# Kernel tuning notes

Hardware: AMD Instinct MI355X
Metric: run time of the kernel (lower is better)

The kernel has to match this reference:

```python
import jax, jax.numpy as jnp
import numpy as np

EMBED_DIM = 2048
NUM_HEADS = 16
HEAD_DIM = EMBED_DIM // NUM_HEADS  # 128
EPS = 1e-12  # F.normalize default eps


def setup_inputs() -> dict:
    key = jax.random.key(0)
    k1, k2, k3 = jax.random.split(key, 3)
    x = jax.random.normal(k1, (4, 2048, EMBED_DIM), dtype=jnp.float32)
    # nn.Linear(embed_dim, 3*embed_dim): weight [3E, E], bias [3E]
    W = jax.random.normal(k2, (3 * EMBED_DIM, EMBED_DIM), dtype=jnp.float32) * (EMBED_DIM ** -0.5)
    b = jax.random.normal(k3, (3 * EMBED_DIM,), dtype=jnp.float32) * 0.02
    return {"x": x, "W": W, "b": b}


def _l2_normalize(t):
    # matches F.normalize(p=2, dim=-1): t / max(||t||, eps)
    n = jnp.sqrt(jnp.sum(t * t, axis=-1, keepdims=True))
    return t / jnp.maximum(n, EPS)


def reference(x, W, b):
    B, L, E = x.shape
    H, HD = NUM_HEADS, HEAD_DIM
    y = x @ W.T + b  # [B, L, 3E]
    # rearrange '... l (h c) -> ... h l c' with c = 3*HD, then chunk into q,k,v
    y = y.reshape(B, L, H, 3, HD)
    q = jnp.transpose(y[..., 0, :], (0, 2, 1, 3))  # [B, H, L, HD]
    k = jnp.transpose(y[..., 1, :], (0, 2, 1, 3))
    v = jnp.transpose(y[..., 2, :], (0, 2, 1, 3))
    q = _l2_normalize(q)
    k = _l2_normalize(k)
    # cosine attention, scale=1, non-causal, no mask
    scores = jnp.einsum('bhld,bhmd->bhlm', q, k)
    attn = jax.nn.softmax(scores, axis=-1)
    out = jnp.einsum('bhlm,bhmd->bhld', attn, v)  # [B, H, L, HD]
    return jnp.transpose(out, (0, 2, 1, 3)).reshape(B, L, E)
```

## Files before the change

kernel.cpp:

```cpp
#include <hip/hip_runtime.h>
#include <hip/hip_bf16.h>

typedef __bf16 bf16_t;
typedef __bf16 bf16x8 __attribute__((ext_vector_type(8)));
typedef __bf16 bf16x4 __attribute__((ext_vector_type(4)));
typedef __bf16 bf16x2 __attribute__((ext_vector_type(2)));
typedef float f32x4 __attribute__((ext_vector_type(4)));

#define MFMA16(a,b,c) __builtin_amdgcn_mfma_f32_16x16x32_bf16((a),(b),(c),0,0,0)
#define AS3(p) ((__attribute__((address_space(3))) void*)(p))
#define AS1(p) ((const __attribute__((address_space(1))) void*)(p))

constexpr int B_ = 4, L_ = 2048, E_ = 2048, H_ = 16, HD_ = 128;
constexpr size_t QK_ELEMS = (size_t)B_ * H_ * L_ * HD_;
constexpr size_t NX = (size_t)B_ * L_ * E_;
constexpr size_t NW = (size_t)3 * E_ * E_;

__global__ __launch_bounds__(256) void cvt(
    const float* __restrict__ X, const float* __restrict__ W, bf16_t* __restrict__ dst)
{
  size_t e = ((size_t)blockIdx.x * 256 + threadIdx.x) * 4;
  f32x4 v = (e < NX) ? *(const f32x4*)&X[e] : *(const f32x4*)&W[e - NX];
  bf16x4 o;
  for (int u = 0; u < 4; ++u) o[u] = (__bf16)v[u];
  *(bf16x4*)&dst[e] = o;
}

__global__ __launch_bounds__(256) void gemm_qkv(
    const bf16_t* __restrict__ Xb, const bf16_t* __restrict__ Wb, const float* __restrict__ bias,
    bf16_t* __restrict__ q, bf16_t* __restrict__ k, bf16_t* __restrict__ vT)
{
  __shared__ alignas(16) bf16_t As[2][128 * 32];
  __shared__ alignas(16) bf16_t Bs[2][128 * 32];
  const int tid = threadIdx.x;
  const int wave = tid >> 6, lane = tid & 63;
  const int wm = wave >> 1, wn = wave & 1;
  const int m0 = blockIdx.y * 128, n0 = blockIdx.x * 128;

  const int sr = lane & 15, sq8 = (lane >> 4) * 8;
  const bf16_t* gA = &Xb[(size_t)(m0 + wave * 32 + sr) * E_ + sq8];
  const bf16_t* gB = &Wb[(size_t)(n0 + wave * 32 + sr) * E_ + sq8];
  bf16_t* lA = &As[0][wave * 1024];
  bf16_t* lB = &Bs[0][wave * 1024];

#define STAGE(c, k0) do { \
    __builtin_amdgcn_global_load_lds(AS1(gA + (k0)),           AS3(lA + (c) * 4096),       16, 0, 0); \
    __builtin_amdgcn_global_load_lds(AS1(gA + 16 * E_ + (k0)), AS3(lA + (c) * 4096 + 512), 16, 0, 0); \
    __builtin_amdgcn_global_load_lds(AS1(gB + (k0)),           AS3(lB + (c) * 4096),       16, 0, 0); \
    __builtin_amdgcn_global_load_lds(AS1(gB + 16 * E_ + (k0)), AS3(lB + (c) * 4096 + 512), 16, 0, 0); \
  } while (0)

  const f32x4 fzero = {0.f, 0.f, 0.f, 0.f};
  f32x4 acc[4][4];
  for (int i = 0; i < 4; ++i)
    for (int j = 0; j < 4; ++j) acc[i][j] = fzero;

  STAGE(0, 0);
  __syncthreads();
  int cur = 0;
  for (int t = 0; t < 64; ++t) {
    if (t < 63) STAGE(cur ^ 1, (t + 1) * 32);
    bf16x8 af[4], bfr[4];
    for (int mt = 0; mt < 4; ++mt) af[mt]  = *(const bf16x8*)&As[cur][(wm * 4 + mt) * 512 + lane * 8];
    for (int nt = 0; nt < 4; ++nt) bfr[nt] = *(const bf16x8*)&Bs[cur][(wn * 4 + nt) * 512 + lane * 8];
    __builtin_amdgcn_s_setprio(1);
    for (int mt = 0; mt < 4; ++mt)
      for (int nt = 0; nt < 4; ++nt)
        acc[mt][nt] = MFMA16(af[mt], bfr[nt], acc[mt][nt]);
    __builtin_amdgcn_s_setprio(0);
    __syncthreads();
    cur ^= 1;
  }
#undef STAGE

  const int b  = m0 >> 11;
  const int l0 = m0 & (L_ - 1);
  const int h  = n0 / 384;
  const int which = (n0 % 384) >> 7;
  const int rlane = (lane >> 4) << 2;
  const int clane = lane & 15;

  float bcol[4];
  for (int nt = 0; nt < 4; ++nt)
    bcol[nt] = bias[n0 + wn * 64 + nt * 16 + clane];

  if (which < 2) {
    float* NormS = (float*)&As[0][0];
    for (int mt = 0; mt < 4; ++mt)
      for (int r = 0; r < 4; ++r) {
        float sq = 0.f;
        for (int nt = 0; nt < 4; ++nt) {
          float v = acc[mt][nt][r] + bcol[nt];
          acc[mt][nt][r] = v;
          sq += v * v;
        }
        for (int off = 8; off; off >>= 1) sq += __shfl_xor(sq, off);
        if (clane == 0) NormS[(wm * 64 + mt * 16 + rlane + r) * 2 + wn] = sq;
      }
    __syncthreads();
    float invn[4][4];
    for (int mt = 0; mt < 4; ++mt)
      for (int r = 0; r < 4; ++r) {
        int ll = wm * 64 + mt * 16 + rlane + r;
        float tot = NormS[ll * 2] + NormS[ll * 2 + 1];
        invn[mt][r] = 1.0f / fmaxf(sqrtf(tot), 1e-12f);
      }
    bf16_t* base = ((which == 0) ? q : k) + ((size_t)(b * H_ + h) * L_) * HD_;
    for (int mt = 0; mt < 4; ++mt)
      for (int r = 0; r < 4; ++r) {
        int l = l0 + wm * 64 + mt * 16 + rlane + r;
        bf16_t* rowp = base + (size_t)l * HD_;
        for (int nt = 0; nt < 4; ++nt) {
          int hd = wn * 64 + nt * 16 + clane;
          rowp[hd] = (__bf16)(acc[mt][nt][r] * invn[mt][r]);
        }
      }
  } else {
    bf16_t* base = vT + ((size_t)(b * H_ + h) * HD_) * L_;
    for (int mt = 0; mt < 4; ++mt)
      for (int r = 0; r < 4; ++r) {
        int l = l0 + wm * 64 + mt * 16 + rlane + r;
        for (int nt = 0; nt < 4; ++nt) {
          int hd = wn * 64 + nt * 16 + clane;
          base[(size_t)hd * L_ + l] = (__bf16)(acc[mt][nt][r] + bcol[nt]);
        }
      }
  }
}

__device__ __forceinline__ int swz128(int r, int c) {
  return r * 128 + ((((c >> 3) ^ (r & 15)) & 15) << 3) + (c & 7);
}
__device__ __forceinline__ int swz64(int r, int c) {
  return r * 64 + ((((c >> 3) ^ (r & 7)) & 7) << 3) + (c & 7);
}

__global__ __launch_bounds__(256) void attn(
    const bf16_t* __restrict__ q, const bf16_t* __restrict__ k,
    const bf16_t* __restrict__ vT, float* __restrict__ out)
{
  __shared__ alignas(16) bf16_t Ks[64 * 128];
  __shared__ alignas(16) bf16_t Vts[128 * 64];
  __shared__ alignas(16) bf16_t Ps[128 * 64];

  const int tid = threadIdx.x, wave = tid >> 6, lane = tid & 63;
  const int bh = blockIdx.y;
  const int q0 = blockIdx.x * 128;
  const int rowf = lane & 15, kq8 = (lane >> 4) * 8;

  const bf16_t* qbase = q + ((size_t)bh * L_ + q0) * HD_;
  const bf16_t* kbh = k + (size_t)bh * L_ * HD_;
  const bf16_t* vbh = vT + (size_t)bh * HD_ * L_;

  bf16x8 qf[4][2];
  for (int kk4 = 0; kk4 < 4; ++kk4)
    for (int mt = 0; mt < 2; ++mt)
      qf[kk4][mt] = *(const bf16x8*)&qbase[(size_t)(wave * 32 + mt * 16 + rowf) * HD_ + kk4 * 32 + kq8];

  const f32x4 fzero = {0.f, 0.f, 0.f, 0.f};
  f32x4 o[2][8];
  for (int mt = 0; mt < 2; ++mt)
    for (int nt = 0; nt < 8; ++nt) o[mt][nt] = fzero;
  float lrow[2][4];
  for (int mt = 0; mt < 2; ++mt)
    for (int r = 0; r < 4; ++r) lrow[mt][r] = 0.f;

  bf16x8 kreg[4], vreg[4];

  for (int i = 0; i < 4; ++i) {
    int e = (i * 256 + tid) * 8;
    kreg[i] = *(const bf16x8*)&kbh[e];
  }
  for (int i = 0; i < 4; ++i) {
    int e = (i * 256 + tid) * 8;
    int d = e >> 6, c = e & 63;
    vreg[i] = *(const bf16x8*)&vbh[(size_t)d * L_ + c];
  }
  for (int i = 0; i < 4; ++i) {
    int e = (i * 256 + tid) * 8;
    *(bf16x8*)&Ks[swz128(e >> 7, e & 127)] = kreg[i];
  }
  for (int i = 0; i < 4; ++i) {
    int e = (i * 256 + tid) * 8;
    int d = e >> 6, c = e & 63;
    *(bf16x8*)&Vts[swz64(d, c)] = vreg[i];
  }
  __syncthreads();

  for (int j0 = 0; j0 < L_; j0 += 64) {
    const bool more = (j0 + 64 < L_);
    if (more) {
      const int jn = j0 + 64;
      for (int i = 0; i < 4; ++i) {
        int e = (i * 256 + tid) * 8;
        kreg[i] = *(const bf16x8*)&kbh[(size_t)jn * HD_ + e];
      }
      for (int i = 0; i < 4; ++i) {
        int e = (i * 256 + tid) * 8;
        int d = e >> 6, c = e & 63;
        vreg[i] = *(const bf16x8*)&vbh[(size_t)d * L_ + jn + c];
      }
    }

    f32x4 s[2][4];
    for (int mt = 0; mt < 2; ++mt)
      for (int nt = 0; nt < 4; ++nt) s[mt][nt] = fzero;
    __builtin_amdgcn_s_setprio(1);
    for (int kk = 0; kk < 128; kk += 32) {
      bf16x8 bk4[4];
      for (int nt = 0; nt < 4; ++nt) bk4[nt] = *(const bf16x8*)&Ks[swz128(nt * 16 + rowf, kk + kq8)];
      for (int mt = 0; mt < 2; ++mt)
        for (int nt = 0; nt < 4; ++nt)
          s[mt][nt] = MFMA16(qf[kk >> 5][mt], bk4[nt], s[mt][nt]);
    }
    __builtin_amdgcn_s_setprio(0);

    for (int mt = 0; mt < 2; ++mt)
      for (int nt = 0; nt < 4; ++nt)
        for (int r = 0; r < 4; ++r) {
          float p = __expf(s[mt][nt][r]);
          lrow[mt][r] += p;
          int rr = wave * 32 + mt * 16 + ((lane >> 4) << 2) + r;
          int cc = nt * 16 + (lane & 15);
          Ps[swz64(rr, cc)] = (__bf16)p;
        }

    __builtin_amdgcn_s_setprio(1);
    for (int kk = 0; kk < 64; kk += 32) {
      bf16x8 ap[2];
      for (int mt = 0; mt < 2; ++mt)
        ap[mt] = *(const bf16x8*)&Ps[swz64(wave * 32 + mt * 16 + rowf, kk + kq8)];
      for (int nt = 0; nt < 8; ++nt) {
        bf16x8 bvv = *(const bf16x8*)&Vts[swz64(nt * 16 + rowf, kk + kq8)];
        for (int mt = 0; mt < 2; ++mt)
          o[mt][nt] = MFMA16(ap[mt], bvv, o[mt][nt]);
      }
    }
    __builtin_amdgcn_s_setprio(0);

    __syncthreads();
    if (more) {
      for (int i = 0; i < 4; ++i) {
        int e = (i * 256 + tid) * 8;
        *(bf16x8*)&Ks[swz128(e >> 7, e & 127)] = kreg[i];
      }
      for (int i = 0; i < 4; ++i) {
        int e = (i * 256 + tid) * 8;
        int d = e >> 6, c = e & 63;
        *(bf16x8*)&Vts[swz64(d, c)] = vreg[i];
      }
      __syncthreads();
    }
  }

  const int b = bh >> 4, h = bh & 15;
  for (int mt = 0; mt < 2; ++mt) {
    for (int r = 0; r < 4; ++r) {
      float lsum = lrow[mt][r];
      for (int off = 8; off; off >>= 1) lsum += __shfl_xor(lsum, off);
      float inv = 1.0f / lsum;
      int l = q0 + wave * 32 + mt * 16 + ((lane >> 4) << 2) + r;
      float* op = out + (((size_t)b * L_ + l) * H_ + h) * HD_;
      for (int nt = 0; nt < 8; ++nt) {
        int d = nt * 16 + (lane & 15);
        op[d] = o[mt][nt][r] * inv;
      }
    }
  }
}

extern "C" void kernel_launch(void* const* d_in, const int* in_sizes, int n_in,
                              void* d_out, int out_size, void* d_ws, size_t ws_size,
                              hipStream_t stream)
{
  const float* X    = (const float*)d_in[0];
  const float* W    = (const float*)d_in[1];
  const float* bias = (const float*)d_in[2];
  float* out = (float*)d_out;

  bf16_t* Xb = (bf16_t*)d_out;
  bf16_t* Wb = Xb + NX;

  bf16_t* q  = (bf16_t*)d_ws;
  bf16_t* k  = q + QK_ELEMS;
  bf16_t* vT = k + QK_ELEMS;

  cvt<<<dim3((NX + NW) / (256 * 4)), 256, 0, stream>>>(X, W, Xb);
  gemm_qkv<<<dim3(48, 64), 256, 0, stream>>>(Xb, Wb, bias, q, k, vT);
  attn<<<dim3(16, 64), 256, 0, stream>>>(q, k, vT, out);
}
```

Measured before the change: 780.3 us.

## Retile QKV GEMM to 256x256x64 blocks with swizzled LDS and deeper prefetch

```diff
diff --git a/kernel.cpp b/kernel.cpp
--- a/kernel.cpp
+++ b/kernel.cpp
@@ -26,103 +26,172 @@
   *(bf16x4*)&dst[e] = o;
 }
 
-__global__ __launch_bounds__(256) void gemm_qkv(
+constexpr int BM = 256, BN = 256, BK = 64, KTILES = E_ / BK;
+
+__global__ __launch_bounds__(512, 2) void gemm_qkv(
     const bf16_t* __restrict__ Xb, const bf16_t* __restrict__ Wb, const float* __restrict__ bias,
     bf16_t* __restrict__ q, bf16_t* __restrict__ k, bf16_t* __restrict__ vT)
 {
-  __shared__ alignas(16) bf16_t As[2][128 * 32];
-  __shared__ alignas(16) bf16_t Bs[2][128 * 32];
+  __shared__ alignas(16) bf16_t Al[2][BM * BK];
+  __shared__ alignas(16) bf16_t Bl[2][BN * BK];
   const int tid = threadIdx.x;
   const int wave = tid >> 6, lane = tid & 63;
-  const int wm = wave >> 1, wn = wave & 1;
-  const int m0 = blockIdx.y * 128, n0 = blockIdx.x * 128;
-
-  const int sr = lane & 15, sq8 = (lane >> 4) * 8;
-  const bf16_t* gA = &Xb[(size_t)(m0 + wave * 32 + sr) * E_ + sq8];
-  const bf16_t* gB = &Wb[(size_t)(n0 + wave * 32 + sr) * E_ + sq8];
-  bf16_t* lA = &As[0][wave * 1024];
-  bf16_t* lB = &Bs[0][wave * 1024];
-
-#define STAGE(c, k0) do { \
-    __builtin_amdgcn_global_load_lds(AS1(gA + (k0)),           AS3(lA + (c) * 4096),       16, 0, 0); \
-    __builtin_amdgcn_global_load_lds(AS1(gA + 16 * E_ + (k0)), AS3(lA + (c) * 4096 + 512), 16, 0, 0); \
-    __builtin_amdgcn_global_load_lds(AS1(gB + (k0)),           AS3(lB + (c) * 4096),       16, 0, 0); \
-    __builtin_amdgcn_global_load_lds(AS1(gB + 16 * E_ + (k0)), AS3(lB + (c) * 4096 + 512), 16, 0, 0); \
+  const int wm = wave >> 2, wn = wave & 3;
+
+  const int bid = blockIdx.y * 24 + blockIdx.x;
+  const int swz = (bid & 7) * 96 + (bid >> 3);
+  const int bx = swz % 24, by = swz / 24;
+  const int m0 = by * BM, n0 = bx * BN;
+
+  const int r8 = lane >> 3;
+  const int cSrc = (lane & 7) ^ r8;
+  const bf16_t* gA = &Xb[(size_t)(m0 + wave * 8 + r8) * E_ + cSrc * 8];
+  const bf16_t* gB = &Wb[(size_t)(n0 + wave * 8 + r8) * E_ + cSrc * 8];
+
+#define STAGE(buf, t) do { \
+    const bf16_t* sa_ = gA + (t) * BK; \
+    const bf16_t* sb_ = gB + (t) * BK; \
+    bf16_t* la_ = &Al[buf][wave * 512]; \
+    bf16_t* lb_ = &Bl[buf][wave * 512]; \
+    __builtin_amdgcn_global_load_lds(AS1(sa_),                       AS3(la_),         16, 0, 0); \
+    __builtin_amdgcn_global_load_lds(AS1(sa_ + (size_t)64 * E_),     AS3(la_ +  4096), 16, 0, 0); \
+    __builtin_amdgcn_global_load_lds(AS1(sa_ + (size_t)128 * E_),    AS3(la_ +  8192), 16, 0, 0); \
+    __builtin_amdgcn_global_load_lds(AS1(sa_ + (size_t)192 * E_),    AS3(la_ + 12288), 16, 0, 0); \
+    __builtin_amdgcn_global_load_lds(AS1(sb_),                       AS3(lb_),         16, 0, 0); \
+    __builtin_amdgcn_global_load_lds(AS1(sb_ + (size_t)64 * E_),     AS3(lb_ +  4096), 16, 0, 0); \
+    __builtin_amdgcn_global_load_lds(AS1(sb_ + (size_t)128 * E_),    AS3(lb_ +  8192), 16, 0, 0); \
+    __builtin_amdgcn_global_load_lds(AS1(sb_ + (size_t)192 * E_),    AS3(lb_ + 12288), 16, 0, 0); \
   } while (0)
 
+  const int rowf = lane & 15, q4 = lane >> 4, rkey = lane & 7;
+#define RD_A(buf, mtg, ks) (*(const bf16x8*)&Al[buf][(wm * 128 + (mtg) * 16 + rowf) * 64 + ((((ks) << 2) | q4) ^ rkey) * 8])
+#define RD_B(buf, nt, ks)  (*(const bf16x8*)&Bl[buf][(wn * 64  + (nt) * 16 + rowf) * 64 + ((((ks) << 2) | q4) ^ rkey) * 8])
+#define SBAR() __builtin_amdgcn_s_barrier()
+
   const f32x4 fzero = {0.f, 0.f, 0.f, 0.f};
-  f32x4 acc[4][4];
-  for (int i = 0; i < 4; ++i)
+  f32x4 acc[8][4];
+#pragma unroll
+  for (int i = 0; i < 8; ++i)
+#pragma unroll
     for (int j = 0; j < 4; ++j) acc[i][j] = fzero;
 
   STAGE(0, 0);
+  STAGE(1, 1);
+  asm volatile("s_waitcnt vmcnt(8)" ::: "memory");
+  SBAR();
+
+  for (int t = 0; t < KTILES; ++t) {
+    const int cur = t & 1;
+    bf16x8 bfr[4][2];
+#pragma unroll
+    for (int p = 0; p < 4; ++p) {
+      bf16x8 af[2][2];
+#pragma unroll
+      for (int i = 0; i < 2; ++i)
+#pragma unroll
+        for (int ks = 0; ks < 2; ++ks)
+          af[i][ks] = RD_A(cur, p * 2 + i, ks);
+      if (p == 0) {
+#pragma unroll
+        for (int nt = 0; nt < 4; ++nt)
+#pragma unroll
+          for (int ks = 0; ks < 2; ++ks)
+            bfr[nt][ks] = RD_B(cur, nt, ks);
+      }
+      SBAR();
+      __builtin_amdgcn_s_setprio(1);
+#pragma unroll
+      for (int i = 0; i < 2; ++i)
+#pragma unroll
+        for (int nt = 0; nt < 4; ++nt)
+#pragma unroll
+          for (int ks = 0; ks < 2; ++ks)
+            acc[p * 2 + i][nt] = MFMA16(af[i][ks], bfr[nt][ks], acc[p * 2 + i][nt]);
+      __builtin_amdgcn_s_setprio(0);
+      if (p < 3) SBAR();
+    }
+    asm volatile("s_waitcnt lgkmcnt(0)" ::: "memory");
+    SBAR();
+    if (t + 2 < KTILES) {
+      STAGE(cur, t + 2);
+      asm volatile("s_waitcnt vmcnt(8)" ::: "memory");
+    } else {
+      asm volatile("s_waitcnt vmcnt(0)" ::: "memory");
+    }
+    SBAR();
+  }
+#undef STAGE
+#undef RD_A
+#undef RD_B
+
   __syncthreads();
-  int cur = 0;
-  for (int t = 0; t < 64; ++t) {
-    if (t < 63) STAGE(cur ^ 1, (t + 1) * 32);
-    bf16x8 af[4], bfr[4];
-    for (int mt = 0; mt < 4; ++mt) af[mt]  = *(const bf16x8*)&As[cur][(wm * 4 + mt) * 512 + lane * 8];
-    for (int nt = 0; nt < 4; ++nt) bfr[nt] = *(const bf16x8*)&Bs[cur][(wn * 4 + nt) * 512 + lane * 8];
-    __builtin_amdgcn_s_setprio(1);
-    for (int mt = 0; mt < 4; ++mt)
-      for (int nt = 0; nt < 4; ++nt)
-        acc[mt][nt] = MFMA16(af[mt], bfr[nt], acc[mt][nt]);
-    __builtin_amdgcn_s_setprio(0);
-    __syncthreads();
-    cur ^= 1;
-  }
-#undef STAGE
 
   const int b  = m0 >> 11;
   const int l0 = m0 & (L_ - 1);
-  const int h  = n0 / 384;
-  const int which = (n0 % 384) >> 7;
+  const int gch = 2 * bx + (wn >> 1);
+  const int h   = gch / 3;
+  const int which = gch % 3;
   const int rlane = (lane >> 4) << 2;
   const int clane = lane & 15;
 
   float bcol[4];
+#pragma unroll
   for (int nt = 0; nt < 4; ++nt)
     bcol[nt] = bias[n0 + wn * 64 + nt * 16 + clane];
-
+#pragma unroll
+  for (int mt = 0; mt < 8; ++mt)
+#pragma unroll
+    for (int nt = 0; nt < 4; ++nt)
+#pragma unroll
+      for (int r = 0; r < 4; ++r)
+        acc[mt][nt][r] += bcol[nt];
+
+  float* NormS = (float*)&Al[0][0];
   if (which < 2) {
-    float* NormS = (float*)&As[0][0];
-    for (int mt = 0; mt < 4; ++mt)
+#pragma unroll
+    for (int mt = 0; mt < 8; ++mt)
+#pragma unroll
       for (int r = 0; r < 4; ++r) {
         float sq = 0.f;
+#pragma unroll
+        for (int nt = 0; nt < 4; ++nt) sq += acc[mt][nt][r] * acc[mt][nt][r];
+#pragma unroll
+        for (int off = 8; off; off >>= 1) sq += __shfl_xor(sq, off);
+        if (clane == 0) {
+          int row = wm * 128 + mt * 16 + rlane + r;
+          NormS[((wn >> 1) * 256 + row) * 2 + (wn & 1)] = sq;
+        }
+      }
+  }
+  __syncthreads();
+
+  if (which < 2) {
+    bf16_t* base = ((which == 0) ? q : k) + ((size_t)(b * H_ + h) * L_) * HD_;
+#pragma unroll
+    for (int mt = 0; mt < 8; ++mt)
+#pragma unroll
+      for (int r = 0; r < 4; ++r) {
+        int row = wm * 128 + mt * 16 + rlane + r;
+        float tot = NormS[((wn >> 1) * 256 + row) * 2] + NormS[((wn >> 1) * 256 + row) * 2 + 1];
+        float invn = 1.0f / fmaxf(sqrtf(tot), 1e-12f);
+        bf16_t* rowp = base + (size_t)(l0 + row) * HD_;
+#pragma unroll
         for (int nt = 0; nt < 4; ++nt) {
-          float v = acc[mt][nt][r] + bcol[nt];
-          acc[mt][nt][r] = v;
-          sq += v * v;
-        }
-        for (int off = 8; off; off >>= 1) sq += __shfl_xor(sq, off);
-        if (clane == 0) NormS[(wm * 64 + mt * 16 + rlane + r) * 2 + wn] = sq;
-      }
-    __syncthreads();
-    float invn[4][4];
-    for (int mt = 0; mt < 4; ++mt)
-      for (int r = 0; r < 4; ++r) {
-        int ll = wm * 64 + mt * 16 + rlane + r;
-        float tot = NormS[ll * 2] + NormS[ll * 2 + 1];
-        invn[mt][r] = 1.0f / fmaxf(sqrtf(tot), 1e-12f);
-      }
-    bf16_t* base = ((which == 0) ? q : k) + ((size_t)(b * H_ + h) * L_) * HD_;
-    for (int mt = 0; mt < 4; ++mt)
-      for (int r = 0; r < 4; ++r) {
-        int l = l0 + wm * 64 + mt * 16 + rlane + r;
-        bf16_t* rowp = base + (size_t)l * HD_;
-        for (int nt = 0; nt < 4; ++nt) {
-          int hd = wn * 64 + nt * 16 + clane;
-          rowp[hd] = (__bf16)(acc[mt][nt][r] * invn[mt][r]);
+          int hd = (wn & 1) * 64 + nt * 16 + clane;
+          rowp[hd] = (__bf16)(acc[mt][nt][r] * invn);
         }
       }
   } else {
     bf16_t* base = vT + ((size_t)(b * H_ + h) * HD_) * L_;
-    for (int mt = 0; mt < 4; ++mt)
+#pragma unroll
+    for (int mt = 0; mt < 8; ++mt)
+#pragma unroll
       for (int r = 0; r < 4; ++r) {
-        int l = l0 + wm * 64 + mt * 16 + rlane + r;
+        int l = l0 + wm * 128 + mt * 16 + rlane + r;
+#pragma unroll
         for (int nt = 0; nt < 4; ++nt) {
-          int hd = wn * 64 + nt * 16 + clane;
-          base[(size_t)hd * L_ + l] = (__bf16)(acc[mt][nt][r] + bcol[nt]);
+          int hd = (wn & 1) * 64 + nt * 16 + clane;
+          base[(size_t)hd * L_ + l] = (__bf16)acc[mt][nt][r];
         }
       }
   }
@@ -286,6 +355,6 @@
   bf16_t* vT = k + QK_ELEMS;
 
   cvt<<<dim3((NX + NW) / (256 * 4)), 256, 0, stream>>>(X, W, Xb);
-  gemm_qkv<<<dim3(48, 64), 256, 0, stream>>>(Xb, Wb, bias, q, k, vT);
+  gemm_qkv<<<dim3(24, 32), 512, 0, stream>>>(Xb, Wb, bias, q, k, vT);
   attn<<<dim3(16, 64), 256, 0, stream>>>(q, k, vT, out);
 }
```

Result: faster. 637.0 us (-18.4%).
